# Kernel tuning notes

Hardware: AMD Instinct MI355X
Metric: run time of the kernel (lower is better)

The kernel has to match this reference:

```python
import math
import jax, jax.numpy as jnp
import numpy as np

NEG = -1e32
H = 8          # n_heads
L2 = 1e-05


def _ln(x, g, b):
    m = jnp.mean(x, -1, keepdims=True)
    v = jnp.mean((x - m) ** 2, -1, keepdims=True)
    return g * (x - m) * jax.lax.rsqrt(v + 1e-5) + b


def _attn(q, k, v, gam, mask_k, zero_pad):
    # q,k,v: [B,H,S,d]; monotonic distance-decay attention (AKT style)
    d_k = q.shape[-1]
    S = q.shape[2]
    scores = jnp.einsum('bhqd,bhkd->bhqk', q, k) / math.sqrt(d_k)
    # torch: triu(ones, k=mask)==0  ->  tril(0) if mask_k==1 else tril(-1)
    mask = jnp.tril(jnp.ones((S, S), bool), 0 if mask_k == 1 else -1)[None, None]
    # first (detached) softmax, used only to build the distance effect
    s_ = jax.nn.softmax(jnp.where(mask, scores, NEG), -1) * mask
    distcum = jnp.cumsum(s_, -1)
    disttot = jnp.sum(s_, -1, keepdims=True)
    idx = jnp.arange(S, dtype=jnp.float32)
    pos = jnp.abs(idx[None, :] - idx[:, None])[None, None]  # |j - i|
    dist = jax.lax.stop_gradient(
        jnp.sqrt(jnp.clip((disttot - distcum) * pos, 0.0, None)))
    gamma = -jax.nn.softplus(gam)[None]  # [1,H,1,1], gam is learned
    total_effect = jnp.clip(jnp.exp(dist * gamma), 1e-5, 1e5)
    scores = jax.nn.softmax(jnp.where(mask, scores * total_effect, NEG), -1)
    if zero_pad:
        scores = scores.at[:, :, 0, :].set(0.0)
    return jnp.einsum('bhqk,bhkd->bhqd', scores, v)


def _mha(qi, ki, vi, kW, kb, vW, vb, oW, ob, gam, mask_k, zero_pad):
    # kq_same=True: q and k both use k_linear
    B, S = qi.shape[:2]
    sp = lambda x: x.reshape(B, S, H, -1).transpose(0, 2, 1, 3)
    q = sp(qi @ kW + kb)
    k = sp(ki @ kW + kb)
    v = sp(vi @ vW + vb)
    o = _attn(q, k, v, gam, mask_k, zero_pad)
    o = o.transpose(0, 2, 1, 3).reshape(B, S, -1)
    return o @ oW + ob


def _tlayer(query, key, values, mask_k, zero_pad, apply_pos,
            kW, kb, vW, vb, oW, ob, gam, ln1g, ln1b,
            f1W, f1b, f2W, f2b, ln2g, ln2b):
    q2 = _mha(query, key, values, kW, kb, vW, vb, oW, ob, gam, mask_k, zero_pad)
    x = _ln(query + q2, ln1g, ln1b)
    if apply_pos:
        ff = jax.nn.relu(x @ f1W + f1b) @ f2W + f2b
        x = _ln(x + ff, ln2g, ln2b)
    return x


def _forward(p_data, pa_data, target, pemb_W, diff_W, qemb_W, qemb_b,
             y_kW, y_kb, y_vW, y_vb, y_oW, y_ob, y_gam, y_ln1g, y_ln1b,
             y_f1W, y_f1b, y_f2W, y_f2b, y_ln2g, y_ln2b,
             x_kW, x_kb, x_vW, x_vb, x_oW, x_ob, x_gam, x_ln1g, x_ln1b,
             h_kW, h_kb, h_vW, h_vb, h_oW, h_ob, h_gam, h_ln1g, h_ln1b,
             h_f1W, h_f1b, h_f2W, h_f2b, h_ln2g, h_ln2b,
             oln1g, oln1b, o1W, o1b, oln2g, oln2b, o2W, o2b,
             oln3g, oln3b, o3W, o3b):
    NPID = pemb_W.shape[0] - 1

    def qe(qd):  # q_embed: Linear -> ReLU, normalized by row-sum of q_data
        return jax.nn.relu(qd @ qemb_W + qemb_b) / jnp.sum(qd, -1, keepdims=True)

    q_data = jax.nn.sigmoid(pemb_W[p_data])           # [B,S,NQ+1]
    q_embed = qe(q_data)                              # [B,S,D]
    pa_pos = jnp.where(pa_data > NPID, pa_data - NPID, 0)
    pa_neg = jnp.where(pa_data <= NPID, pa_data, 0)
    qa_pos = jax.nn.sigmoid(pemb_W[pa_pos])
    qa_neg = jax.nn.sigmoid(pemb_W[pa_neg])
    qa_embed = jnp.concatenate([qe(qa_pos), qe(qa_neg)], -1)  # [B,S,2D]
    pid = diff_W[p_data]                              # [B,S,1]
    q_embed = q_embed + pid
    qa_embed = qa_embed + pid
    c_reg = jnp.sum(pid ** 2) * L2

    # Architecture (n_blocks = 1)
    y = _tlayer(qa_embed, qa_embed, qa_embed, 1, False, True,
                y_kW, y_kb, y_vW, y_vb, y_oW, y_ob, y_gam, y_ln1g, y_ln1b,
                y_f1W, y_f1b, y_f2W, y_f2b, y_ln2g, y_ln2b)
    x = _tlayer(q_embed, q_embed, q_embed, 1, False, False,
                x_kW, x_kb, x_vW, x_vb, x_oW, x_ob, x_gam, x_ln1g, x_ln1b,
                None, None, None, None, None, None)
    x = _tlayer(x, x, y, 0, True, True,
                h_kW, h_kb, h_vW, h_vb, h_oW, h_ob, h_gam, h_ln1g, h_ln1b,
                h_f1W, h_f1b, h_f2W, h_f2b, h_ln2g, h_ln2b)

    c = jnp.concatenate([x, q_embed], -1)             # [B,S,2D]
    o = jax.nn.relu(_ln(c, oln1g, oln1b) @ o1W + o1b)
    o = jax.nn.relu(_ln(o, oln2g, oln2b) @ o2W + o2b)
    out = _ln(o, oln3g, oln3b) @ o3W + o3b            # [B,S,1]
    return out, c_reg


def setup_inputs():
    B, S, D, NQ, NPID, FC, DFF = 8, 1024, 256, 1024, 4096, 512, 2048
    key = jax.random.key(0)
    cnt = [0]

    def nk():
        cnt[0] += 1
        return jax.random.fold_in(key, cnt[0])

    def nrm(shape, s=0.05):
        return jax.random.normal(nk(), shape, dtype=jnp.float32) * s

    z = lambda sh: jnp.zeros(sh, jnp.float32)
    on = lambda sh: jnp.ones(sh, jnp.float32)

    return dict(
        p_data=jax.random.randint(nk(), (B, S), 0, NPID + 1),
        pa_data=jax.random.randint(nk(), (B, S), 0, 2 * NPID + 1),
        target=jax.random.uniform(nk(), (B, S), jnp.float32),
        pemb_W=nrm((NPID + 1, NQ + 1), 1.0), diff_W=nrm((NPID + 1, 1), 0.1),
        qemb_W=nrm((NQ + 1, D)), qemb_b=z((D,)),
        y_kW=nrm((2 * D, 2 * D)), y_kb=z((2 * D,)),
        y_vW=nrm((2 * D, 2 * D)), y_vb=z((2 * D,)),
        y_oW=nrm((2 * D, 2 * D)), y_ob=z((2 * D,)), y_gam=nrm((H, 1, 1), 1.0),
        y_ln1g=on((2 * D,)), y_ln1b=z((2 * D,)),
        y_f1W=nrm((2 * D, DFF)), y_f1b=z((DFF,)),
        y_f2W=nrm((DFF, 2 * D)), y_f2b=z((2 * D,)),
        y_ln2g=on((2 * D,)), y_ln2b=z((2 * D,)),
        x_kW=nrm((D, D)), x_kb=z((D,)), x_vW=nrm((D, D)), x_vb=z((D,)),
        x_oW=nrm((D, D)), x_ob=z((D,)), x_gam=nrm((H, 1, 1), 1.0),
        x_ln1g=on((D,)), x_ln1b=z((D,)),
        h_kW=nrm((D, D)), h_kb=z((D,)),
        h_vW=nrm((2 * D, 2 * D)), h_vb=z((2 * D,)),
        h_oW=nrm((2 * D, D)), h_ob=z((D,)), h_gam=nrm((H, 1, 1), 1.0),
        h_ln1g=on((D,)), h_ln1b=z((D,)),
        h_f1W=nrm((D, DFF)), h_f1b=z((DFF,)),
        h_f2W=nrm((DFF, D)), h_f2b=z((D,)),
        h_ln2g=on((D,)), h_ln2b=z((D,)),
        oln1g=on((2 * D,)), oln1b=z((2 * D,)),
        o1W=nrm((2 * D, FC)), o1b=z((FC,)),
        oln2g=on((FC,)), oln2b=z((FC,)),
        o2W=nrm((FC, 256)), o2b=z((256,)),
        oln3g=on((256,)), oln3b=z((256,)),
        o3W=nrm((256, 1)), o3b=z((1,)),
    )


def reference(p_data, pa_data, target, pemb_W, diff_W, qemb_W, qemb_b,
              y_kW, y_kb, y_vW, y_vb, y_oW, y_ob, y_gam, y_ln1g, y_ln1b,
              y_f1W, y_f1b, y_f2W, y_f2b, y_ln2g, y_ln2b,
              x_kW, x_kb, x_vW, x_vb, x_oW, x_ob, x_gam, x_ln1g, x_ln1b,
              h_kW, h_kb, h_vW, h_vb, h_oW, h_ob, h_gam, h_ln1g, h_ln1b,
              h_f1W, h_f1b, h_f2W, h_f2b, h_ln2g, h_ln2b,
              oln1g, oln1b, o1W, o1b, oln2g, oln2b, o2W, o2b,
              oln3g, oln3b, o3W, o3b):
    return _forward(p_data, pa_data, target, pemb_W, diff_W, qemb_W, qemb_b,
                    y_kW, y_kb, y_vW, y_vb, y_oW, y_ob, y_gam, y_ln1g, y_ln1b,
                    y_f1W, y_f1b, y_f2W, y_f2b, y_ln2g, y_ln2b,
                    x_kW, x_kb, x_vW, x_vb, x_oW, x_ob, x_gam, x_ln1g, x_ln1b,
                    h_kW, h_kb, h_vW, h_vb, h_oW, h_ob, h_gam, h_ln1g, h_ln1b,
                    h_f1W, h_f1b, h_f2W, h_f2b, h_ln2g, h_ln2b,
                    oln1g, oln1b, o1W, o1b, oln2g, oln2b, o2W, o2b,
                    oln3g, oln3b, o3W, o3b)
```

## Files before the change

### kernel.cpp

```cpp
#include <hip/hip_runtime.h>
#include <hip/hip_bf16.h>
#include <math.h>

#define NHEADS 8
#define L2E 1.44269504f

typedef __attribute__((ext_vector_type(8))) __bf16 bfrag;
typedef __attribute__((ext_vector_type(4))) float f32x4;
typedef __attribute__((ext_vector_type(8))) unsigned short u16x8;

static __device__ __forceinline__ unsigned short f2bf(float f) {
  unsigned u = __float_as_uint(f);
  unsigned r = (u + 0x7fffu + ((u >> 16) & 1u)) >> 16;
  return (unsigned short)r;
}

static __device__ __forceinline__ void gload_lds16(const void* g, void* l) {
  __builtin_amdgcn_global_load_lds(
      (const __attribute__((address_space(1))) unsigned int*)g,
      (__attribute__((address_space(3))) unsigned int*)l, 16, 0, 0);
}

static __device__ __forceinline__ float block_reduce_sum(float v, float* red) {
  int t = threadIdx.x;
// ... 15 lines not shown
  int row = blockIdx.x;
  float s = 0.f;
  for (int k = threadIdx.x; k < Kp; k += 256) {
    float v = 0.f;
    if (k < Kd) {
      v = 1.f / (1.f + __expf(-Wp[(size_t)row * Kd + k]));
      s += v;
    }
    Sgb[(size_t)row * Kp + k] = f2bf(v);
  }
  float tot = block_reduce_sum(s, red);
  if (threadIdx.x == 0) Ssum[row] = tot;
}

struct TDesc { const float* src; unsigned short* dst; int K, N, Kp, tilesX, blk0; };
struct TPack { TDesc d[16]; };

__global__ __launch_bounds__(256) void tconv_all_kernel(TPack P) {
  __shared__ float t[32][33];
  int bid = blockIdx.x;
  int di = 0;
  #pragma unroll
  for (int k = 1; k < 16; ++k) if (bid >= P.d[k].blk0) di = k;
  const float* src = P.d[di].src;
  unsigned short* dst = P.d[di].dst;
  int K = P.d[di].K, N = P.d[di].N, Kp = P.d[di].Kp, tilesX = P.d[di].tilesX;
  int local = bid - P.d[di].blk0;
  int bn = (local % tilesX) * 32;
  int bk = (local / tilesX) * 32;
  int tid = threadIdx.x;
  int tx = tid & 31, ty = tid >> 5;
  #pragma unroll
  for (int u = 0; u < 4; ++u) {
    int k = bk + ty + u * 8, n = bn + tx;
    t[ty + u * 8][tx] = (k < K && n < N) ? src[(size_t)k * N + n] : 0.f;
  }
  __syncthreads();
  #pragma unroll
  for (int u = 0; u < 4; ++u) {
    int n = bn + ty + u * 8, kk = bk + tx;
    if (n < N && kk < Kp)
      dst[(size_t)n * Kp + kk] = f2bf(t[tx][ty + u * 8]);
  }
}

template<int BM, int EPI, bool WF32, bool WBF, bool WTR>
__global__ __launch_bounds__(256) void mgemm_kernel(
    const unsigned short* __restrict__ A, const unsigned short* __restrict__ Bt,
    const float* __restrict__ bias, float* __restrict__ C,
    unsigned short* __restrict__ Cb, unsigned short* __restrict__ Ct,
    int M, int N, int K, const float* __restrict__ divv,
    const float* __restrict__ bias2, int Nk)
{
  constexpr int NJ = (BM == 128) ? 4 : 2;
  constexpr bool SPLIT = WBF && WTR;
  __shared__ __align__(16) unsigned short Als[BM * 32];
  __shared__ __align__(16) unsigned short Bls[128 * 32];
  const int tid = threadIdx.x;
  const int lane = tid & 63, w = tid >> 6;
  const int wm = (BM == 128) ? (w >> 1) : 0;
  const int wn = (BM == 128) ? (w & 1) : w;
  const int brow = blockIdx.y * BM, bcol = blockIdx.x * 128;

  f32x4 acc[4][NJ] = {};

  for (int k0 = 0; k0 < K; k0 += 32) {
    #pragma unroll
    for (int q = 0; q < 2; ++q) {
      int s = w * 128 + q * 64 + lane;
      int r = s >> 2, g = s & 3;
      int gs = g ^ (r & 3);
      int gc = bcol + r; if (gc > N - 1) gc = N - 1;
      gload_lds16(Bt + (size_t)gc * K + k0 + gs * 8,
                  (char*)Bls + (w * 2048 + q * 1024));
    }
    if constexpr (BM == 128) {
      #pragma unroll
      for (int q = 0; q < 2; ++q) {
        int s = w * 128 + q * 64 + lane;
        int r = s >> 2, g = s & 3;
        int gs = g ^ (r & 3);
        int gr = brow + r; if (gr > M - 1) gr = M - 1;
        gload_lds16(A + (size_t)gr * K + k0 + gs * 8,
                    (char*)Als + (w * 2048 + q * 1024));
      }
    } else {
      int s = w * 64 + lane;
      int r = s >> 2, g = s & 3;
      int gs = g ^ (r & 3);
      int gr = brow + r; if (gr > M - 1) gr = M - 1;
      gload_lds16(A + (size_t)gr * K + k0 + gs * 8,
                  (char*)Als + w * 1024);
    }
    __syncthreads();

    bfrag av[4], bv[NJ];
    #pragma unroll
    for (int f = 0; f < 4; ++f) {
      int rA = wm * 64 + f * 16 + (lane & 15);
      av[f] = *(const bfrag*)((const char*)Als + rA * 64 + ((((lane >> 4) ^ (rA & 3))) << 4));
    }
    #pragma unroll
    for (int f = 0; f < NJ; ++f) {
      int rB = wn * (16 * NJ) + f * 16 + (lane & 15);
      bv[f] = *(const bfrag*)((const char*)Bls + rB * 64 + ((((lane >> 4) ^ (rB & 3))) << 4));
    }
    #pragma unroll
    for (int i = 0; i < 4; ++i)
      #pragma unroll
      for (int j = 0; j < NJ; ++j)
        acc[i][j] = __builtin_amdgcn_mfma_f32_16x16x32_bf16(av[i], bv[j], acc[i][j], 0, 0, 0);
    __syncthreads();
  }

  #pragma unroll
  for (int i = 0; i < 4; ++i) {
    int gr0 = brow + wm * 64 + i * 16 + (lane >> 4) * 4;
    #pragma unroll
    for (int j = 0; j < NJ; ++j) {
      int gc = bcol + wn * (16 * NJ) + j * 16 + (lane & 15);
      float bsv;
      if (SPLIT) bsv = (gc < Nk) ? bias[gc] : bias2[gc - Nk];
      else       bsv = bias ? bias[gc] : 0.f;
      float vv[4];
      #pragma unroll
      for (int q = 0; q < 4; ++q) {
        int gr = gr0 + q;
        float v = acc[i][j][q] + bsv;
        if (EPI >= 1) v = fmaxf(v, 0.f);
        if (EPI == 2) v = (gr < M) ? v / divv[gr] : v;
        vv[q] = v;
      }
      if (SPLIT) {
        if (gc < Nk) {
          #pragma unroll
          for (int q = 0; q < 4; ++q) {
            int gr = gr0 + q;
            if (gr < M) Cb[(size_t)gr * Nk + gc] = f2bf(vv[q]);
          }
        } else {
          ushort4 h4 = { f2bf(vv[0]), f2bf(vv[1]), f2bf(vv[2]), f2bf(vv[3]) };
          *(ushort4*)(Ct + (size_t)(gc - Nk) * M + gr0) = h4;
        }
      } else {
        #pragma unroll
        for (int q = 0; q < 4; ++q) {
          int gr = gr0 + q;
          if (gr >= M) continue;
          if (WF32) C[(size_t)gr * N + gc] = vv[q];
          if (WBF)  Cb[(size_t)gr * N + gc] = f2bf(vv[q]);
        }
        if (WTR) {
          ushort4 h4 = { f2bf(vv[0]), f2bf(vv[1]), f2bf(vv[2]), f2bf(vv[3]) };
          *(ushort4*)(Ct + (size_t)gc * M + gr0) = h4;
        }
      }
    }
  }
}

__global__ __launch_bounds__(256) void gather_kernel(
    const int* __restrict__ p_data, const int* __restrict__ pa_data,
    const float* __restrict__ E, const float* __restrict__ diff_W,
    float* __restrict__ qemb, unsigned short* __restrict__ qembb,
    float* __restrict__ qaemb, unsigned short* __restrict__ qaembb)
{
  int idx = blockIdx.x * 256 + threadIdx.x;
  if (idx >= 8192 * 512) return;
  int row = idx >> 9, c = idx & 511;
  int p = p_data[row];
  float pid = diff_W[p];
  if (c < 256) {
    float v = E[(size_t)p * 256 + c] + pid;
    qemb[(size_t)row * 256 + c] = v;
    qembb[(size_t)row * 256 + c] = f2bf(v);
  }
  int pa = pa_data[row];
  int ppos = (pa > 4096) ? pa - 4096 : 0;
  int pneg = (pa <= 4096) ? pa : 0;
  float v = (c < 256) ? E[(size_t)ppos * 256 + c] : E[(size_t)pneg * 256 + (c - 256)];
  v += pid;
  qaemb[(size_t)row * 512 + c] = v;
  qaembb[(size_t)row * 512 + c] = f2bf(v);
}

__global__ __launch_bounds__(256) void creg_kernel(
    const int* __restrict__ p_data, const float* __restrict__ dW,
    float* __restrict__ out)
{
  __shared__ float red[256];
  float s = 0.f;
  for (int i = threadIdx.x; i < 8192; i += 256) {
    float v = dW[p_data[i]];
    s += v * v;
  }
  float tot = block_reduce_sum(s, red);
  if (threadIdx.x == 0) out[0] = tot * 1e-5f;
}

template<int DK, int DV, int MASKK, int ZP, int CHUNK>
__global__ __launch_bounds__(512, 4) void attn7_kernel(
    const unsigned short* __restrict__ QKb, const unsigned short* __restrict__ Vt,
    const float* __restrict__ gamp, unsigned short* __restrict__ O,
    int S, int MT, int bxoff)
{
  constexpr int RS = 36 * CHUNK + 4;
  constexpr int LBITS = (CHUNK == 32) ? 2 : 1;
  constexpr int LM = (1 << LBITS) - 1;
  constexpr int HIOFF = 64 * CHUNK;
  constexpr int NPAR = (DV == 64) ? 2 : 4;
  constexpr int NFIN = (DV == 64) ? 4 : 2;
  constexpr int NP   = (DV == 32) ? 6 : 4;
  constexpr int MAXIT = (DV == 64) ? (CHUNK == 32 ? 8 : 4) : (CHUNK == 32 ? 4 : 2);
  const int DMK = NHEADS * DK, DMV = NHEADS * DV;
  const int nIb = gridDim.x;
  const int id = blockIdx.x + blockIdx.y * nIb;
  const int cpx = nIb * 8;
  const int W = (id & 7) * cpx + (id >> 3);
  const int ib = (nIb - 1) - (W % nIb);
  const int bh = W / nIb;
  const int i0 = (ib + bxoff) * 16;
  const int b = bh >> 3, h = bh & 7;
  const int tid = threadIdx.x;
  const int lane = tid & 63, w = tid >> 6;
  const size_t rowbase = (size_t)b * S;

  __shared__ __align__(16) float sc[16 * RS];
  __shared__ float red[NP * 16 * 17];
  __shared__ float wrow[16];

  const int jmaxBlk = MASKK ? (i0 + 15) : (i0 + 14);
  const int nT = jmaxBlk / 64 + 1;
  const int NK = nT * 64;

  const int qr = lane & 15;
  const int ko8 = (lane >> 4) * 8;
  const float rscale = rsqrtf((float)DK) * L2E;

  const int dblk = (DV == 64) ? (w & 3) : (w & 1);
  const int par  = (DV == 64) ? (w >> 2) : (w >> 1);
  const int dcol = h * DV + dblk * 16 + (lane & 15);
  const unsigned short* vrow = Vt + (size_t)dcol * MT + rowbase;
  bfrag vpre[2 * MAXIT];

  bfrag qf[DK / 32];
  #pragma unroll
  for (int ks = 0; ks < DK / 32; ++ks)
    qf[ks] = *(const bfrag*)(QKb + (rowbase + i0 + qr) * DMK + h * DK + ks * 32 + ko8);

  for (int t0 = 0; t0 < NK; t0 += 128) {
    int tt = t0 + (w >> 2) * 64;
    if (tt < NK) {
      int jb = tt + (w & 3) * 16 + qr;
      bfrag kf[DK / 32];
      #pragma unroll
      for (int ks = 0; ks < DK / 32; ++ks)
        kf[ks] = *(const bfrag*)(QKb + (rowbase + jb) * DMK + h * DK + ks * 32 + ko8);
      f32x4 accs = {};
      #pragma unroll
      for (int ks = 0; ks < DK / 32; ++ks)
        accs = __builtin_amdgcn_mfma_f32_16x16x32_bf16(qf[ks], kf[ks], accs, 0, 0, 0);
      int ja = jb + 4 * (jb >> 5);
      int r0 = (lane >> 4) * 4;
      #pragma unroll
      for (int q = 0; q < 4; ++q)
        sc[(r0 + q) * RS + ja] = accs[q] * rscale;
    }
  }
  __syncthreads();

  {
    const int g = tid >> 5, l = tid & 31;
    const int i = i0 + g;
    const int jmax = MASKK ? i : i - 1;
    const int jb0 = CHUNK * l;
    const int sb = g * RS + jb0 + 4 * (jb0 >> 5);

    float p[CHUNK];
    float m1 = -1e30f;
    #pragma unroll
    for (int c = 0; c < CHUNK / 4; ++c) {
      f32x4 v = *(const f32x4*)(sc + sb + c * 4);
      #pragma unroll
      for (int k = 0; k < 4; ++k) {
        int j = jb0 + c * 4 + k;
        float s = (j <= jmax) ? v[k] : -1e30f;
        p[c * 4 + k] = s;
        m1 = fmaxf(m1, s);
      }
    }
    #pragma unroll
    for (int o = 16; o > 0; o >>= 1) m1 = fmaxf(m1, __shfl_xor(m1, o, 32));

    float e1[CHUNK];
    float lloc = 0.f;
    #pragma unroll
    for (int t = 0; t < CHUNK; ++t) { e1[t] = __builtin_amdgcn_exp2f(p[t] - m1); lloc += e1[t]; }
    float l1 = lloc;
    #pragma unroll
    for (int o = 16; o > 0; o >>= 1) l1 += __shfl_xor(l1, o, 32);

    float scn = lloc;
    #pragma unroll
    for (int o = 1; o < 32; o <<= 1) {
      float u = __shfl_up(scn, o, 32);
      if (l >= o) scn += u;
    }
    float cum = scn - lloc;

    float gv = gamp[h];
    float sp = fmaxf(gv, 0.f) + log1pf(__expf(-fabsf(gv)));
    float gmr = -sp * L2E * rsqrtf(l1);
    float dj = (float)(i - jb0);
    float m2 = -1e30f;
    #pragma unroll
    for (int t = 0; t < CHUNK; ++t) {
      cum += e1[t];
      float rem = fmaxf(l1 - cum, 0.f);
      float dsq = sqrtf(rem * fabsf(dj));
      dj -= 1.f;
      float eff = fmaxf(__builtin_amdgcn_exp2f(gmr * dsq), 1e-5f);
      p[t] = p[t] * eff;
      m2 = fmaxf(m2, p[t]);
    }
    #pragma unroll
    for (int o = 16; o > 0; o >>= 1) m2 = fmaxf(m2, __shfl_xor(m2, o, 32));

    float l2 = 0.f;
    #pragma unroll
    for (int t = 0; t < CHUNK; ++t) { p[t] = __builtin_amdgcn_exp2f(p[t] - m2); l2 += p[t]; }
    #pragma unroll
    for (int o = 16; o > 0; o >>= 1) l2 += __shfl_xor(l2, o, 32);
    bool validrow = (jmax >= 0) && !(ZP && i == 0);
    float wgt = validrow ? (1.f / l2) : 0.f;
    if (l == 0) wrow[g] = wgt;

    #pragma unroll
    for (int it = 0; it < MAXIT; ++it) {
      int t0 = (par + it * NPAR) * 64;
      int t0c = (t0 < NK) ? t0 : 0;
      #pragma unroll
      for (int ks = 0; ks < 2; ++ks)
        vpre[it * 2 + ks] = *(const bfrag*)(vrow + t0c + ks * 32 + ko8);
    }

    char* rowB = (char*)sc + (size_t)g * (RS * 4);
    #pragma unroll
    for (int k = 0; k < CHUNK / 8; ++k) {
      int bb = (CHUNK / 8) * l + k;
      int pb = ((bb & LM) << 5) | (bb >> LBITS);
      u16x8 hi8, lo8;
      #pragma unroll
      for (int e = 0; e < 8; ++e) {
        float v = p[8 * k + e];
        __bf16 hb = (__bf16)v;
        hi8[e] = __builtin_bit_cast(unsigned short, hb);
        lo8[e] = __builtin_bit_cast(unsigned short, (__bf16)(v - (float)hb));
      }
      *(u16x8*)(rowB + 16 * pb) = hi8;
      *(u16x8*)(rowB + HIOFF + 16 * pb) = lo8;
    }
  }
  __syncthreads();

  f32x4 acco = {};
  const char* rowB = (const char*)sc + (size_t)qr * (RS * 4);
  #pragma unroll
  for (int it = 0; it < MAXIT; ++it) {
    int t0 = (par + it * NPAR) * 64;
    if (t0 < NK) {
      #pragma unroll
      for (int ks = 0; ks < 2; ++ks) {
        int jo = t0 + ks * 32 + ko8;
        int bb = jo >> 3;
        int pb = ((bb & LM) << 5) | (bb >> LBITS);
        bfrag ph = *(const bfrag*)(rowB + 16 * pb);
        bfrag pl = *(const bfrag*)(rowB + HIOFF + 16 * pb);
        bfrag vf = vpre[it * 2 + ks];
        acco = __builtin_amdgcn_mfma_f32_16x16x32_bf16(pl, vf, acco, 0, 0, 0);
        acco = __builtin_amdgcn_mfma_f32_16x16x32_bf16(ph, vf, acco, 0, 0, 0);
      }
    }
  }

  if (w >= NFIN) {
    #pragma unroll
    for (int q = 0; q < 4; ++q)
      red[(w - NFIN) * 272 + ((lane >> 4) * 4 + q) * 17 + (lane & 15)] = acco[q];
  }
  __syncthreads();
  if (w < NFIN) {
    for (int pp = w; pp < NP; pp += NFIN) {
      #pragma unroll
      for (int q = 0; q < 4; ++q)
        acco[q] += red[pp * 272 + ((lane >> 4) * 4 + q) * 17 + (lane & 15)];
    }
    int r0 = (lane >> 4) * 4;
    #pragma unroll
    for (int q = 0; q < 4; ++q) {
      float wv = wrow[r0 + q];
      O[(rowbase + i0 + r0 + q) * DMV + dcol] = f2bf(acco[q] * wv);
    }
  }
}

template<int D, bool WF, bool WB>
__global__ __launch_bounds__(256) void ln4_kernel(
    const float* __restrict__ X, const float* __restrict__ R,
    const float* __restrict__ g, const float* __restrict__ be,
    float* __restrict__ Y, unsigned short* __restrict__ Yb)
{
  constexpr int NC = D / 256;
  int row = blockIdx.x * 4 + (threadIdx.x >> 6);
  int lane = threadIdx.x & 63;
  const float* x = X + (size_t)row * D;
  f32x4 xv[NC];
  float s = 0.f;
  #pragma unroll
  for (int c = 0; c < NC; ++c) {
    xv[c] = *(const f32x4*)(x + c * 256 + lane * 4);
    if (R) {
      f32x4 rv = *(const f32x4*)(R + (size_t)row * D + c * 256 + lane * 4);
      #pragma unroll
      for (int k = 0; k < 4; ++k) xv[c][k] += rv[k];
    }
    #pragma unroll
    for (int k = 0; k < 4; ++k) s += xv[c][k];
  }
  #pragma unroll
  for (int o = 32; o > 0; o >>= 1) s += __shfl_xor(s, o, 64);
  float mean = s / (float)D;
  float vs = 0.f;
  #pragma unroll
  for (int c = 0; c < NC; ++c)
    #pragma unroll
    for (int k = 0; k < 4; ++k) { float d = xv[c][k] - mean; vs += d * d; }
  #pragma unroll
  for (int o = 32; o > 0; o >>= 1) vs += __shfl_xor(vs, o, 64);
  float rstd = rsqrtf(vs / (float)D + 1e-5f);
  #pragma unroll
  for (int c = 0; c < NC; ++c) {
    f32x4 gv = *(const f32x4*)(g + c * 256 + lane * 4);
    f32x4 bv = *(const f32x4*)(be + c * 256 + lane * 4);
    f32x4 ov;
    #pragma unroll
    for (int k = 0; k < 4; ++k) ov[k] = gv[k] * (xv[c][k] - mean) * rstd + bv[k];
    if (WF) *(f32x4*)(Y + (size_t)row * D + c * 256 + lane * 4) = ov;
    if (WB) {
// ... 167 lines not shown
  float* XO   = ws + oXO;   unsigned short* XOb = (unsigned short*)(ws + oXOb);
  float* HO   = ws + oHO;
  float* S0   = ws + oS0;
  unsigned short* S2b = (unsigned short*)(ws + oS2b);
  float* S3   = ws + oS3;
  float* S4   = ws + oS4;
  float* SX   = ws + oSX;   unsigned short* SXb = (unsigned short*)(ws + oSXb);
  unsigned short* S0b = (unsigned short*)(ws + oS0b);
  unsigned short* Vt  = (unsigned short*)(ws + oVt);
  unsigned short* FFb = (unsigned short*)S0;

  unsigned short* Wqe  = (unsigned short*)(ws + oWqe);
  unsigned short* Wyk  = (unsigned short*)(ws + oWyk);
  unsigned short* Wyv  = (unsigned short*)(ws + oWyv);
  unsigned short* Wyo  = (unsigned short*)(ws + oWyo);
  unsigned short* Wyf1 = (unsigned short*)(ws + oWyf1);
  unsigned short* Wyf2 = (unsigned short*)(ws + oWyf2);
  unsigned short* Wxk  = (unsigned short*)(ws + oWxk);
  unsigned short* Wxv  = (unsigned short*)(ws + oWxv);
  unsigned short* Wxo  = (unsigned short*)(ws + oWxo);
  unsigned short* Whk  = (unsigned short*)(ws + oWhk);
  unsigned short* Whv  = (unsigned short*)(ws + oWhv);
  unsigned short* Who  = (unsigned short*)(ws + oWho);
  unsigned short* Whf1 = (unsigned short*)(ws + oWhf1);
  unsigned short* Whf2 = (unsigned short*)(ws + oWhf2);
  unsigned short* Wo1  = (unsigned short*)(ws + oWo1);
  unsigned short* Wo2  = (unsigned short*)(ws + oWo2);

  dim3 blk(256);
  int nElem512 = (8192 * 512 + 255) / 256;

  {
    struct HD { const float* src; unsigned short* dst; int K, N, Kp; };
    const HD hd[16] = {
      {qemb_W, Wqe, KQ, 256, KQP},
      {y_kW, Wyk, 512, 512, 512}, {y_vW, Wyv, 512, 512, 512}, {y_oW, Wyo, 512, 512, 512},
      {y_f1W, Wyf1, 512, 2048, 512}, {y_f2W, Wyf2, 2048, 512, 2048},
      {x_kW, Wxk, 256, 256, 256}, {x_vW, Wxv, 256, 256, 256}, {x_oW, Wxo, 256, 256, 256},
      {h_kW, Whk, 256, 256, 256}, {h_vW, Whv, 512, 512, 512}, {h_oW, Who, 512, 256, 512},
      {h_f1W, Whf1, 256, 2048, 256}, {h_f2W, Whf2, 2048, 256, 2048},
      {o1W, Wo1, 512, 512, 512}, {o2W, Wo2, 512, 256, 512},
    };
    TPack P;
    int tot = 0;
    for (int k = 0; k < 16; ++k) {
      int tx = (hd[k].N + 31) / 32, ty = (hd[k].Kp + 31) / 32;
      P.d[k] = { hd[k].src, hd[k].dst, hd[k].K, hd[k].N, hd[k].Kp, tx, tot };
      tot += tx * ty;
    }
    tconv_all_kernel<<<dim3(tot), blk, 0, stream>>>(P);
  }

  auto gg128 = [](int Mm, int Nn) { return dim3((unsigned)(Nn / 128), (unsigned)((Mm + 127) / 128)); };
  auto gg64  = [](int Mm, int Nn) { return dim3((unsigned)(Nn / 128), (unsigned)((Mm + 63) / 64)); };

  sig_kernel<<<R, blk, 0, stream>>>(pemb_W, SIGb, SSUM, KQ, KQP);
  mgemm_kernel<64, 2, true, false, false><<<gg64(R, 256), blk, 0, stream>>>(SIGb, Wqe, qemb_b, E, nullptr, nullptr, R, 256, KQP, SSUM, nullptr, 0);
  gather_kernel<<<nElem512, blk, 0, stream>>>(p_data, pa_data, E, diff_W, QE, QEb, QA, QAb);
  creg_kernel<<<1, blk, 0, stream>>>(p_data, diff_W, out_f + 8192);

  dim3 ablk(512);
  dim3 lgrid(M / 4);
  dim3 agB(32, B * NHEADS), agC(32, B * NHEADS);

  mgemm_kernel<128, 0, false, true, true><<<dim3(8, 64), blk, 0, stream>>>(QAb, Wyk, y_kb, nullptr, S0b, Vt, M, 1024, 512, nullptr, y_vb, 512);
  attn7_kernel<64, 64, 1, 0, 16><<<agB, ablk, 0, stream>>>(S0b, Vt, y_gam, S2b, S, M, 0);
  attn7_kernel<64, 64, 1, 0, 32><<<agC, ablk, 0, stream>>>(S0b, Vt, y_gam, S2b, S, M, 32);
  mgemm_kernel<128, 0, true, false, false><<<gg128(M, 512), blk, 0, stream>>>(S2b, Wyo, y_ob, S3, nullptr, nullptr, M, 512, 512, nullptr, nullptr, 0);
  ln4_kernel<512, true, true><<<lgrid, blk, 0, stream>>>(QA, S3, y_ln1g, y_ln1b, SX, SXb);
  mgemm_kernel<128, 1, false, true, false><<<gg128(M, 2048), blk, 0, stream>>>(SXb, Wyf1, y_f1b, nullptr, FFb, nullptr, M, 2048, 512, nullptr, nullptr, 0);
  mgemm_kernel<128, 0, true, false, false><<<gg128(M, 512), blk, 0, stream>>>(FFb, Wyf2, y_f2b, S4, nullptr, nullptr, M, 512, 2048, nullptr, nullptr, 0);
  ln4_kernel<512, false, true><<<lgrid, blk, 0, stream>>>(SX, S4, y_ln2g, y_ln2b, nullptr, YOb);

  mgemm_kernel<128, 0, false, true, true><<<dim3(4, 64), blk, 0, stream>>>(QEb, Wxk, x_kb, nullptr, S0b, Vt, M, 512, 256, nullptr, x_vb, 256);
  attn7_kernel<32, 32, 1, 0, 16><<<agB, ablk, 0, stream>>>(S0b, Vt, x_gam, S2b, S, M, 0);
  attn7_kernel<32, 32, 1, 0, 32><<<agC, ablk, 0, stream>>>(S0b, Vt, x_gam, S2b, S, M, 32);
  mgemm_kernel<64, 0, true, false, false><<<gg64(M, 256), blk, 0, stream>>>(S2b, Wxo, x_ob, S3, nullptr, nullptr, M, 256, 256, nullptr, nullptr, 0);
  ln4_kernel<256, true, true><<<lgrid, blk, 0, stream>>>(QE, S3, x_ln1g, x_ln1b, XO, XOb);

  mgemm_kernel<64, 0, false, true, false><<<gg64(M, 256), blk, 0, stream>>>(XOb, Whk, h_kb, nullptr, S0b, nullptr, M, 256, 256, nullptr, nullptr, 0);
  mgemm_kernel<128, 0, false, false, true><<<gg128(M, 512), blk, 0, stream>>>(YOb, Whv, h_vb, nullptr, nullptr, Vt, M, 512, 512, nullptr, nullptr, 0);
  attn7_kernel<32, 64, 0, 1, 16><<<agB, ablk, 0, stream>>>(S0b, Vt, h_gam, S2b, S, M, 0);
  attn7_kernel<32, 64, 0, 1, 32><<<agC, ablk, 0, stream>>>(S0b, Vt, h_gam, S2b, S, M, 32);
  mgemm_kernel<64, 0, true, false, false><<<gg64(M, 256), blk, 0, stream>>>(S2b, Who, h_ob, S3, nullptr, nullptr, M, 256, 512, nullptr, nullptr, 0);
  ln4_kernel<256, true, true><<<lgrid, blk, 0, stream>>>(XO, S3, h_ln1g, h_ln1b, SX, SXb);
  mgemm_kernel<128, 1, false, true, false><<<gg128(M, 2048), blk, 0, stream>>>(SXb, Whf1, h_f1b, nullptr, FFb, nullptr, M, 2048, 256, nullptr, nullptr, 0);
  mgemm_kernel<64, 0, true, false, false><<<gg64(M, 256), blk, 0, stream>>>(FFb, Whf2, h_f2b, S4, nullptr, nullptr, M, 256, 2048, nullptr, nullptr, 0);
  ln4_kernel<256, true, false><<<lgrid, blk, 0, stream>>>(SX, S4, h_ln2g, h_ln2b, HO, nullptr);

  lnc_kernel<<<lgrid, blk, 0, stream>>>(HO, QE, oln1g, oln1b, SXb);
  mgemm_kernel<128, 1, true, false, false><<<gg128(M, 512), blk, 0, stream>>>(SXb, Wo1, o1b, S3, nullptr, nullptr, M, 512, 512, nullptr, nullptr, 0);
  ln4_kernel<512, false, true><<<lgrid, blk, 0, stream>>>(S3, nullptr, oln2g, oln2b, nullptr, SXb);
  mgemm_kernel<64, 1, true, false, false><<<gg64(M, 256), blk, 0, stream>>>(SXb, Wo2, o2b, S4, nullptr, nullptr, M, 256, 512, nullptr, nullptr, 0);
  lndot_kernel<<<lgrid, blk, 0, stream>>>(S4, oln3g, oln3b, o3W, o3b, out_f);
}
```

Measured before the change: 836.8 us.

## Widen attention blocks to 1024 threads with one wavefront per query row

The attention kernel moves from 512 to 1024 threads per block and assigns a full 64-lane wavefront to each query row, so wave-wide shuffles replace the 32-lane sub-group ones. The score pass and the P·V pass are split across twice as many waves, and the cross-partition reduction reuses the score shared buffer instead of a separate array. V fragments are now loaded inside the MFMA loop rather than prefetched before the softmax, which gives up that overlap in exchange for lower register pressure. The 1024-thread blocks and the extra barrier may reduce occupancy or add synchronization cost.

```diff
diff --git a/kernel.cpp b/kernel.cpp
--- a/kernel.cpp
+++ b/kernel.cpp
@@ -237,20 +237,20 @@
   if (threadIdx.x == 0) out[0] = tot * 1e-5f;
 }
 
-template<int DK, int DV, int MASKK, int ZP, int CHUNK>
-__global__ __launch_bounds__(512, 4) void attn7_kernel(
+template<int DK, int DV, int MASKK, int ZP, int CL>
+__global__ __launch_bounds__(1024, 8) void attn8_kernel(
     const unsigned short* __restrict__ QKb, const unsigned short* __restrict__ Vt,
     const float* __restrict__ gamp, unsigned short* __restrict__ O,
     int S, int MT, int bxoff)
 {
-  constexpr int RS = 36 * CHUNK + 4;
-  constexpr int LBITS = (CHUNK == 32) ? 2 : 1;
-  constexpr int LM = (1 << LBITS) - 1;
-  constexpr int HIOFF = 64 * CHUNK;
-  constexpr int NPAR = (DV == 64) ? 2 : 4;
-  constexpr int NFIN = (DV == 64) ? 4 : 2;
-  constexpr int NP   = (DV == 32) ? 6 : 4;
-  constexpr int MAXIT = (DV == 64) ? (CHUNK == 32 ? 8 : 4) : (CHUNK == 32 ? 4 : 2);
+  constexpr int CHUNK = CL / 64;
+  constexpr int RS = CL + CL / 8 + 4;
+  constexpr int NB = CL / 8;
+  constexpr int LSH = (NB == 128) ? 6 : 5;
+  constexpr int HIOFF = NB * 16;
+  constexpr int NPAR = (DV == 64) ? 4 : 8;
+  constexpr int NDB  = (DV == 64) ? 4 : 2;
+  constexpr int MAXIT = CL / (64 * NPAR);
   const int DMK = NHEADS * DK, DMV = NHEADS * DV;
   const int nIb = gridDim.x;
   const int id = blockIdx.x + blockIdx.y * nIb;
@@ -265,29 +265,21 @@
   const size_t rowbase = (size_t)b * S;
 
   __shared__ __align__(16) float sc[16 * RS];
-  __shared__ float red[NP * 16 * 17];
   __shared__ float wrow[16];
 
   const int jmaxBlk = MASKK ? (i0 + 15) : (i0 + 14);
-  const int nT = jmaxBlk / 64 + 1;
-  const int NK = nT * 64;
+  const int NK = (jmaxBlk / 64 + 1) * 64;
 
   const int qr = lane & 15;
   const int ko8 = (lane >> 4) * 8;
   const float rscale = rsqrtf((float)DK) * L2E;
 
-  const int dblk = (DV == 64) ? (w & 3) : (w & 1);
-  const int par  = (DV == 64) ? (w >> 2) : (w >> 1);
-  const int dcol = h * DV + dblk * 16 + (lane & 15);
-  const unsigned short* vrow = Vt + (size_t)dcol * MT + rowbase;
-  bfrag vpre[2 * MAXIT];
-
   bfrag qf[DK / 32];
   #pragma unroll
   for (int ks = 0; ks < DK / 32; ++ks)
     qf[ks] = *(const bfrag*)(QKb + (rowbase + i0 + qr) * DMK + h * DK + ks * 32 + ko8);
 
-  for (int t0 = 0; t0 < NK; t0 += 128) {
+  for (int t0 = 0; t0 < NK; t0 += 256) {
     int tt = t0 + (w >> 2) * 64;
     if (tt < NK) {
       int jb = tt + (w & 3) * 16 + qr;
@@ -309,7 +301,7 @@
   __syncthreads();
 
   {
-    const int g = tid >> 5, l = tid & 31;
+    const int g = w, l = lane;
     const int i = i0 + g;
     const int jmax = MASKK ? i : i - 1;
     const int jb0 = CHUNK * l;
@@ -329,7 +321,7 @@
       }
     }
     #pragma unroll
-    for (int o = 16; o > 0; o >>= 1) m1 = fmaxf(m1, __shfl_xor(m1, o, 32));
+    for (int o = 32; o > 0; o >>= 1) m1 = fmaxf(m1, __shfl_xor(m1, o, 64));
 
     float e1[CHUNK];
     float lloc = 0.f;
@@ -337,12 +329,12 @@
     for (int t = 0; t < CHUNK; ++t) { e1[t] = __builtin_amdgcn_exp2f(p[t] - m1); lloc += e1[t]; }
     float l1 = lloc;
     #pragma unroll
-    for (int o = 16; o > 0; o >>= 1) l1 += __shfl_xor(l1, o, 32);
+    for (int o = 32; o > 0; o >>= 1) l1 += __shfl_xor(l1, o, 64);
 
     float scn = lloc;
     #pragma unroll
-    for (int o = 1; o < 32; o <<= 1) {
-      float u = __shfl_up(scn, o, 32);
+    for (int o = 1; o < 64; o <<= 1) {
+      float u = __shfl_up(scn, o, 64);
       if (l >= o) scn += u;
     }
     float cum = scn - lloc;
@@ -363,31 +355,22 @@
       m2 = fmaxf(m2, p[t]);
     }
     #pragma unroll
-    for (int o = 16; o > 0; o >>= 1) m2 = fmaxf(m2, __shfl_xor(m2, o, 32));
+    for (int o = 32; o > 0; o >>= 1) m2 = fmaxf(m2, __shfl_xor(m2, o, 64));
 
     float l2 = 0.f;
     #pragma unroll
     for (int t = 0; t < CHUNK; ++t) { p[t] = __builtin_amdgcn_exp2f(p[t] - m2); l2 += p[t]; }
     #pragma unroll
-    for (int o = 16; o > 0; o >>= 1) l2 += __shfl_xor(l2, o, 32);
+    for (int o = 32; o > 0; o >>= 1) l2 += __shfl_xor(l2, o, 64);
     bool validrow = (jmax >= 0) && !(ZP && i == 0);
     float wgt = validrow ? (1.f / l2) : 0.f;
     if (l == 0) wrow[g] = wgt;
 
-    #pragma unroll
-    for (int it = 0; it < MAXIT; ++it) {
-      int t0 = (par + it * NPAR) * 64;
-      int t0c = (t0 < NK) ? t0 : 0;
-      #pragma unroll
-      for (int ks = 0; ks < 2; ++ks)
-        vpre[it * 2 + ks] = *(const bfrag*)(vrow + t0c + ks * 32 + ko8);
-    }
-
     char* rowB = (char*)sc + (size_t)g * (RS * 4);
     #pragma unroll
     for (int k = 0; k < CHUNK / 8; ++k) {
       int bb = (CHUNK / 8) * l + k;
-      int pb = ((bb & LM) << 5) | (bb >> LBITS);
+      int pb = ((bb & 1) << LSH) | (bb >> 1);
       u16x8 hi8, lo8;
       #pragma unroll
       for (int e = 0; e < 8; ++e) {
@@ -402,6 +385,10 @@
   }
   __syncthreads();
 
+  const int dblk = (DV == 64) ? (w & 3) : (w & 1);
+  const int par  = (DV == 64) ? (w >> 2) : (w >> 1);
+  const int dcol = h * DV + dblk * 16 + (lane & 15);
+  const unsigned short* vrow = Vt + (size_t)dcol * MT + rowbase;
   f32x4 acco = {};
   const char* rowB = (const char*)sc + (size_t)qr * (RS * 4);
   #pragma unroll
@@ -412,27 +399,32 @@
       for (int ks = 0; ks < 2; ++ks) {
         int jo = t0 + ks * 32 + ko8;
         int bb = jo >> 3;
-        int pb = ((bb & LM) << 5) | (bb >> LBITS);
+        int pb = ((bb & 1) << LSH) | (bb >> 1);
         bfrag ph = *(const bfrag*)(rowB + 16 * pb);
         bfrag pl = *(const bfrag*)(rowB + HIOFF + 16 * pb);
-        bfrag vf = vpre[it * 2 + ks];
+        bfrag vf = *(const bfrag*)(vrow + jo);
         acco = __builtin_amdgcn_mfma_f32_16x16x32_bf16(pl, vf, acco, 0, 0, 0);
         acco = __builtin_amdgcn_mfma_f32_16x16x32_bf16(ph, vf, acco, 0, 0, 0);
       }
     }
   }
-
-  if (w >= NFIN) {
+  __syncthreads();
+
+  float* redA = sc;
+  if (par != 0) {
+    int slot = (par - 1) * NDB + dblk;
     #pragma unroll
     for (int q = 0; q < 4; ++q)
-      red[(w - NFIN) * 272 + ((lane >> 4) * 4 + q) * 17 + (lane & 15)] = acco[q];
+      redA[slot * 272 + ((lane >> 4) * 4 + q) * 17 + (lane & 15)] = acco[q];
   }
   __syncthreads();
-  if (w < NFIN) {
-    for (int pp = w; pp < NP; pp += NFIN) {
+  if (par == 0) {
+    #pragma unroll
+    for (int pp = 1; pp < NPAR; ++pp) {
+      int slot = (pp - 1) * NDB + dblk;
       #pragma unroll
       for (int q = 0; q < 4; ++q)
-        acco[q] += red[pp * 272 + ((lane >> 4) * 4 + q) * 17 + (lane & 15)];
+        acco[q] += redA[slot * 272 + ((lane >> 4) * 4 + q) * 17 + (lane & 15)];
     }
     int r0 = (lane >> 4) * 4;
     #pragma unroll
@@ -713,13 +705,13 @@
   gather_kernel<<<nElem512, blk, 0, stream>>>(p_data, pa_data, E, diff_W, QE, QEb, QA, QAb);
   creg_kernel<<<1, blk, 0, stream>>>(p_data, diff_W, out_f + 8192);
 
-  dim3 ablk(512);
+  dim3 ablk(1024);
   dim3 lgrid(M / 4);
   dim3 agB(32, B * NHEADS), agC(32, B * NHEADS);
 
   mgemm_kernel<128, 0, false, true, true><<<dim3(8, 64), blk, 0, stream>>>(QAb, Wyk, y_kb, nullptr, S0b, Vt, M, 1024, 512, nullptr, y_vb, 512);
-  attn7_kernel<64, 64, 1, 0, 16><<<agB, ablk, 0, stream>>>(S0b, Vt, y_gam, S2b, S, M, 0);
-  attn7_kernel<64, 64, 1, 0, 32><<<agC, ablk, 0, stream>>>(S0b, Vt, y_gam, S2b, S, M, 32);
+  attn8_kernel<64, 64, 1, 0, 512><<<agB, ablk, 0, stream>>>(S0b, Vt, y_gam, S2b, S, M, 0);
+  attn8_kernel<64, 64, 1, 0, 1024><<<agC, ablk, 0, stream>>>(S0b, Vt, y_gam, S2b, S, M, 32);
   mgemm_kernel<128, 0, true, false, false><<<gg128(M, 512), blk, 0, stream>>>(S2b, Wyo, y_ob, S3, nullptr, nullptr, M, 512, 512, nullptr, nullptr, 0);
   ln4_kernel<512, true, true><<<lgrid, blk, 0, stream>>>(QA, S3, y_ln1g, y_ln1b, SX, SXb);
   mgemm_kernel<128, 1, false, true, false><<<gg128(M, 2048), blk, 0, stream>>>(SXb, Wyf1, y_f1b, nullptr, FFb, nullptr, M, 2048, 512, nullptr, nullptr, 0);
@@ -727,15 +719,15 @@
   ln4_kernel<512, false, true><<<lgrid, blk, 0, stream>>>(SX, S4, y_ln2g, y_ln2b, nullptr, YOb);
 
   mgemm_kernel<128, 0, false, true, true><<<dim3(4, 64), blk, 0, stream>>>(QEb, Wxk, x_kb, nullptr, S0b, Vt, M, 512, 256, nullptr, x_vb, 256);
-  attn7_kernel<32, 32, 1, 0, 16><<<agB, ablk, 0, stream>>>(S0b, Vt, x_gam, S2b, S, M, 0);
-  attn7_kernel<32, 32, 1, 0, 32><<<agC, ablk, 0, stream>>>(S0b, Vt, x_gam, S2b, S, M, 32);
+  attn8_kernel<32, 32, 1, 0, 512><<<agB, ablk, 0, stream>>>(S0b, Vt, x_gam, S2b, S, M, 0);
+  attn8_kernel<32, 32, 1, 0, 1024><<<agC, ablk, 0, stream>>>(S0b, Vt, x_gam, S2b, S, M, 32);
   mgemm_kernel<64, 0, true, false, false><<<gg64(M, 256), blk, 0, stream>>>(S2b, Wxo, x_ob, S3, nullptr, nullptr, M, 256, 256, nullptr, nullptr, 0);
   ln4_kernel<256, true, true><<<lgrid, blk, 0, stream>>>(QE, S3, x_ln1g, x_ln1b, XO, XOb);
 
   mgemm_kernel<64, 0, false, true, false><<<gg64(M, 256), blk, 0, stream>>>(XOb, Whk, h_kb, nullptr, S0b, nullptr, M, 256, 256, nullptr, nullptr, 0);
   mgemm_kernel<128, 0, false, false, true><<<gg128(M, 512), blk, 0, stream>>>(YOb, Whv, h_vb, nullptr, nullptr, Vt, M, 512, 512, nullptr, nullptr, 0);
-  attn7_kernel<32, 64, 0, 1, 16><<<agB, ablk, 0, stream>>>(S0b, Vt, h_gam, S2b, S, M, 0);
-  attn7_kernel<32, 64, 0, 1, 32><<<agC, ablk, 0, stream>>>(S0b, Vt, h_gam, S2b, S, M, 32);
+  attn8_kernel<32, 64, 0, 1, 512><<<agB, ablk, 0, stream>>>(S0b, Vt, h_gam, S2b, S, M, 0);
+  attn8_kernel<32, 64, 0, 1, 1024><<<agC, ablk, 0, stream>>>(S0b, Vt, h_gam, S2b, S, M, 32);
   mgemm_kernel<64, 0, true, false, false><<<gg64(M, 256), blk, 0, stream>>>(S2b, Who, h_ob, S3, nullptr, nullptr, M, 256, 512, nullptr, nullptr, 0);
   ln4_kernel<256, true, true><<<lgrid, blk, 0, stream>>>(XO, S3, h_ln1g, h_ln1b, SX, SXb);
   mgemm_kernel<128, 1, false, true, false><<<gg128(M, 2048), blk, 0, stream>>>(SXb, Whf1, h_f1b, nullptr, FFb, nullptr, M, 2048, 256, nullptr, nullptr, 0);
```

After: 844.2 us. About the same (+0.9%).

## Use 64x64 GEMM tiles and cut attention register pressure for higher occupancy

Applied to the files above, without the earlier changes.

The BM=64 GEMM variant now uses a 64x64 tile with a 2x2 warp grid instead of 64x128, doubling the grid size for the N=256 GEMMs. The attention kernel drops the e1[] array (recomputing exp2) and the V prefetch registers, loads V inside the loop, and reuses the score shared buffer for the cross-warp reduction. This lets it declare 8 waves-per-SIMD occupancy for CHUNK=16. The aim is more resident blocks and better latency hiding, paid for with extra exp2 work and V loads that are no longer prefetched.

```diff
diff --git a/kernel.cpp b/kernel.cpp
--- a/kernel.cpp
+++ b/kernel.cpp
@@ -91,29 +91,31 @@
     int M, int N, int K, const float* __restrict__ divv,
     const float* __restrict__ bias2, int Nk)
 {
-  constexpr int NJ = (BM == 128) ? 4 : 2;
+  constexpr int TN  = (BM == 128) ? 128 : 64;
+  constexpr int NI  = (BM == 128) ? 4 : 2;
+  constexpr int NJ  = (BM == 128) ? 4 : 2;
+  constexpr int WSM = (BM == 128) ? 64 : 32;
   constexpr bool SPLIT = WBF && WTR;
   __shared__ __align__(16) unsigned short Als[BM * 32];
-  __shared__ __align__(16) unsigned short Bls[128 * 32];
+  __shared__ __align__(16) unsigned short Bls[TN * 32];
   const int tid = threadIdx.x;
   const int lane = tid & 63, w = tid >> 6;
-  const int wm = (BM == 128) ? (w >> 1) : 0;
-  const int wn = (BM == 128) ? (w & 1) : w;
-  const int brow = blockIdx.y * BM, bcol = blockIdx.x * 128;
-
-  f32x4 acc[4][NJ] = {};
+  const int wm = w >> 1, wn = w & 1;
+  const int brow = blockIdx.y * BM, bcol = blockIdx.x * TN;
+
+  f32x4 acc[NI][NJ] = {};
 
   for (int k0 = 0; k0 < K; k0 += 32) {
-    #pragma unroll
-    for (int q = 0; q < 2; ++q) {
-      int s = w * 128 + q * 64 + lane;
-      int r = s >> 2, g = s & 3;
-      int gs = g ^ (r & 3);
-      int gc = bcol + r; if (gc > N - 1) gc = N - 1;
-      gload_lds16(Bt + (size_t)gc * K + k0 + gs * 8,
-                  (char*)Bls + (w * 2048 + q * 1024));
-    }
     if constexpr (BM == 128) {
+      #pragma unroll
+      for (int q = 0; q < 2; ++q) {
+        int s = w * 128 + q * 64 + lane;
+        int r = s >> 2, g = s & 3;
+        int gs = g ^ (r & 3);
+        int gc = bcol + r; if (gc > N - 1) gc = N - 1;
+        gload_lds16(Bt + (size_t)gc * K + k0 + gs * 8,
+                    (char*)Bls + (w * 2048 + q * 1024));
+      }
       #pragma unroll
       for (int q = 0; q < 2; ++q) {
         int s = w * 128 + q * 64 + lane;
@@ -124,28 +126,38 @@
                     (char*)Als + (w * 2048 + q * 1024));
       }
     } else {
-      int s = w * 64 + lane;
-      int r = s >> 2, g = s & 3;
-      int gs = g ^ (r & 3);
-      int gr = brow + r; if (gr > M - 1) gr = M - 1;
-      gload_lds16(A + (size_t)gr * K + k0 + gs * 8,
-                  (char*)Als + w * 1024);
+      {
+        int s = tid;
+        int r = s >> 2, g = s & 3;
+        int gs = g ^ (r & 3);
+        int gc = bcol + r; if (gc > N - 1) gc = N - 1;
+        gload_lds16(Bt + (size_t)gc * K + k0 + gs * 8,
+                    (char*)Bls + w * 1024);
+      }
+      {
+        int s = tid;
+        int r = s >> 2, g = s & 3;
+        int gs = g ^ (r & 3);
+        int gr = brow + r; if (gr > M - 1) gr = M - 1;
+        gload_lds16(A + (size_t)gr * K + k0 + gs * 8,
+                    (char*)Als + w * 1024);
+      }
     }
     __syncthreads();
 
-    bfrag av[4], bv[NJ];
-    #pragma unroll
-    for (int f = 0; f < 4; ++f) {
-      int rA = wm * 64 + f * 16 + (lane & 15);
+    bfrag av[NI], bv[NJ];
+    #pragma unroll
+    for (int f = 0; f < NI; ++f) {
+      int rA = wm * WSM + f * 16 + (lane & 15);
       av[f] = *(const bfrag*)((const char*)Als + rA * 64 + ((((lane >> 4) ^ (rA & 3))) << 4));
     }
     #pragma unroll
     for (int f = 0; f < NJ; ++f) {
-      int rB = wn * (16 * NJ) + f * 16 + (lane & 15);
+      int rB = wn * WSM + f * 16 + (lane & 15);
       bv[f] = *(const bfrag*)((const char*)Bls + rB * 64 + ((((lane >> 4) ^ (rB & 3))) << 4));
     }
     #pragma unroll
-    for (int i = 0; i < 4; ++i)
+    for (int i = 0; i < NI; ++i)
       #pragma unroll
       for (int j = 0; j < NJ; ++j)
         acc[i][j] = __builtin_amdgcn_mfma_f32_16x16x32_bf16(av[i], bv[j], acc[i][j], 0, 0, 0);
@@ -153,11 +165,11 @@
   }
 
   #pragma unroll
-  for (int i = 0; i < 4; ++i) {
-    int gr0 = brow + wm * 64 + i * 16 + (lane >> 4) * 4;
+  for (int i = 0; i < NI; ++i) {
+    int gr0 = brow + wm * WSM + i * 16 + (lane >> 4) * 4;
     #pragma unroll
     for (int j = 0; j < NJ; ++j) {
-      int gc = bcol + wn * (16 * NJ) + j * 16 + (lane & 15);
+      int gc = bcol + wn * WSM + j * 16 + (lane & 15);
       float bsv;
       if (SPLIT) bsv = (gc < Nk) ? bias[gc] : bias2[gc - Nk];
       else       bsv = bias ? bias[gc] : 0.f;
@@ -238,7 +250,7 @@
 }
 
 template<int DK, int DV, int MASKK, int ZP, int CHUNK>
-__global__ __launch_bounds__(512, 4) void attn7_kernel(
+__global__ __launch_bounds__(512, (CHUNK == 16) ? 8 : 4) void attn9_kernel(
     const unsigned short* __restrict__ QKb, const unsigned short* __restrict__ Vt,
     const float* __restrict__ gamp, unsigned short* __restrict__ O,
     int S, int MT, int bxoff)
@@ -250,7 +262,6 @@
   constexpr int NPAR = (DV == 64) ? 2 : 4;
   constexpr int NFIN = (DV == 64) ? 4 : 2;
   constexpr int NP   = (DV == 32) ? 6 : 4;
-  constexpr int MAXIT = (DV == 64) ? (CHUNK == 32 ? 8 : 4) : (CHUNK == 32 ? 4 : 2);
   const int DMK = NHEADS * DK, DMV = NHEADS * DV;
   const int nIb = gridDim.x;
   const int id = blockIdx.x + blockIdx.y * nIb;
@@ -265,22 +276,14 @@
   const size_t rowbase = (size_t)b * S;
 
   __shared__ __align__(16) float sc[16 * RS];
-  __shared__ float red[NP * 16 * 17];
   __shared__ float wrow[16];
 
   const int jmaxBlk = MASKK ? (i0 + 15) : (i0 + 14);
-  const int nT = jmaxBlk / 64 + 1;
-  const int NK = nT * 64;
+  const int NK = (jmaxBlk / 64 + 1) * 64;
 
   const int qr = lane & 15;
   const int ko8 = (lane >> 4) * 8;
   const float rscale = rsqrtf((float)DK) * L2E;
-
-  const int dblk = (DV == 64) ? (w & 3) : (w & 1);
-  const int par  = (DV == 64) ? (w >> 2) : (w >> 1);
-  const int dcol = h * DV + dblk * 16 + (lane & 15);
-  const unsigned short* vrow = Vt + (size_t)dcol * MT + rowbase;
-  bfrag vpre[2 * MAXIT];
 
   bfrag qf[DK / 32];
   #pragma unroll
@@ -331,10 +334,9 @@
     #pragma unroll
     for (int o = 16; o > 0; o >>= 1) m1 = fmaxf(m1, __shfl_xor(m1, o, 32));
 
-    float e1[CHUNK];
     float lloc = 0.f;
     #pragma unroll
-    for (int t = 0; t < CHUNK; ++t) { e1[t] = __builtin_amdgcn_exp2f(p[t] - m1); lloc += e1[t]; }
+    for (int t = 0; t < CHUNK; ++t) lloc += __builtin_amdgcn_exp2f(p[t] - m1);
     float l1 = lloc;
     #pragma unroll
     for (int o = 16; o > 0; o >>= 1) l1 += __shfl_xor(l1, o, 32);
@@ -354,7 +356,7 @@
     float m2 = -1e30f;
     #pragma unroll
     for (int t = 0; t < CHUNK; ++t) {
-      cum += e1[t];
+      cum += __builtin_amdgcn_exp2f(p[t] - m1);
       float rem = fmaxf(l1 - cum, 0.f);
       float dsq = sqrtf(rem * fabsf(dj));
       dj -= 1.f;
@@ -373,15 +375,6 @@
     bool validrow = (jmax >= 0) && !(ZP && i == 0);
     float wgt = validrow ? (1.f / l2) : 0.f;
     if (l == 0) wrow[g] = wgt;
-
-    #pragma unroll
-    for (int it = 0; it < MAXIT; ++it) {
-      int t0 = (par + it * NPAR) * 64;
-      int t0c = (t0 < NK) ? t0 : 0;
-      #pragma unroll
-      for (int ks = 0; ks < 2; ++ks)
-        vpre[it * 2 + ks] = *(const bfrag*)(vrow + t0c + ks * 32 + ko8);
-    }
 
     char* rowB = (char*)sc + (size_t)g * (RS * 4);
     #pragma unroll
@@ -402,37 +395,40 @@
   }
   __syncthreads();
 
+  const int dblk = (DV == 64) ? (w & 3) : (w & 1);
+  const int par  = (DV == 64) ? (w >> 2) : (w >> 1);
+  const int dcol = h * DV + dblk * 16 + (lane & 15);
+  const unsigned short* vrow = Vt + (size_t)dcol * MT + rowbase;
   f32x4 acco = {};
   const char* rowB = (const char*)sc + (size_t)qr * (RS * 4);
-  #pragma unroll
-  for (int it = 0; it < MAXIT; ++it) {
-    int t0 = (par + it * NPAR) * 64;
-    if (t0 < NK) {
-      #pragma unroll
-      for (int ks = 0; ks < 2; ++ks) {
-        int jo = t0 + ks * 32 + ko8;
-        int bb = jo >> 3;
-        int pb = ((bb & LM) << 5) | (bb >> LBITS);
-        bfrag ph = *(const bfrag*)(rowB + 16 * pb);
-        bfrag pl = *(const bfrag*)(rowB + HIOFF + 16 * pb);
-        bfrag vf = vpre[it * 2 + ks];
-        acco = __builtin_amdgcn_mfma_f32_16x16x32_bf16(pl, vf, acco, 0, 0, 0);
-        acco = __builtin_amdgcn_mfma_f32_16x16x32_bf16(ph, vf, acco, 0, 0, 0);
-      }
-    }
-  }
-
+  for (int t0 = par * 64; t0 < NK; t0 += NPAR * 64) {
+    #pragma unroll
+    for (int ks = 0; ks < 2; ++ks) {
+      int jo = t0 + ks * 32 + ko8;
+      int bb = jo >> 3;
+      int pb = ((bb & LM) << 5) | (bb >> LBITS);
+      bfrag ph = *(const bfrag*)(rowB + 16 * pb);
+      bfrag pl = *(const bfrag*)(rowB + HIOFF + 16 * pb);
+      bfrag vf = *(const bfrag*)(vrow + jo);
+      acco = __builtin_amdgcn_mfma_f32_16x16x32_bf16(pl, vf, acco, 0, 0, 0);
+      acco = __builtin_amdgcn_mfma_f32_16x16x32_bf16(ph, vf, acco, 0, 0, 0);
+    }
+  }
+  __syncthreads();
+
+  float* redA = sc;
   if (w >= NFIN) {
+    int slot = w - NFIN;
     #pragma unroll
     for (int q = 0; q < 4; ++q)
-      red[(w - NFIN) * 272 + ((lane >> 4) * 4 + q) * 17 + (lane & 15)] = acco[q];
+      redA[slot * 272 + ((lane >> 4) * 4 + q) * 17 + (lane & 15)] = acco[q];
   }
   __syncthreads();
   if (w < NFIN) {
     for (int pp = w; pp < NP; pp += NFIN) {
       #pragma unroll
       for (int q = 0; q < 4; ++q)
-        acco[q] += red[pp * 272 + ((lane >> 4) * 4 + q) * 17 + (lane & 15)];
+        acco[q] += redA[pp * 272 + ((lane >> 4) * 4 + q) * 17 + (lane & 15)];
     }
     int r0 = (lane >> 4) * 4;
     #pragma unroll
@@ -706,7 +702,7 @@
   }
 
   auto gg128 = [](int Mm, int Nn) { return dim3((unsigned)(Nn / 128), (unsigned)((Mm + 127) / 128)); };
-  auto gg64  = [](int Mm, int Nn) { return dim3((unsigned)(Nn / 128), (unsigned)((Mm + 63) / 64)); };
+  auto gg64  = [](int Mm, int Nn) { return dim3((unsigned)(Nn / 64), (unsigned)((Mm + 63) / 64)); };
 
   sig_kernel<<<R, blk, 0, stream>>>(pemb_W, SIGb, SSUM, KQ, KQP);
   mgemm_kernel<64, 2, true, false, false><<<gg64(R, 256), blk, 0, stream>>>(SIGb, Wqe, qemb_b, E, nullptr, nullptr, R, 256, KQP, SSUM, nullptr, 0);
@@ -718,8 +714,8 @@
   dim3 agB(32, B * NHEADS), agC(32, B * NHEADS);
 
   mgemm_kernel<128, 0, false, true, true><<<dim3(8, 64), blk, 0, stream>>>(QAb, Wyk, y_kb, nullptr, S0b, Vt, M, 1024, 512, nullptr, y_vb, 512);
-  attn7_kernel<64, 64, 1, 0, 16><<<agB, ablk, 0, stream>>>(S0b, Vt, y_gam, S2b, S, M, 0);
-  attn7_kernel<64, 64, 1, 0, 32><<<agC, ablk, 0, stream>>>(S0b, Vt, y_gam, S2b, S, M, 32);
+  attn9_kernel<64, 64, 1, 0, 16><<<agB, ablk, 0, stream>>>(S0b, Vt, y_gam, S2b, S, M, 0);
+  attn9_kernel<64, 64, 1, 0, 32><<<agC, ablk, 0, stream>>>(S0b, Vt, y_gam, S2b, S, M, 32);
   mgemm_kernel<128, 0, true, false, false><<<gg128(M, 512), blk, 0, stream>>>(S2b, Wyo, y_ob, S3, nullptr, nullptr, M, 512, 512, nullptr, nullptr, 0);
   ln4_kernel<512, true, true><<<lgrid, blk, 0, stream>>>(QA, S3, y_ln1g, y_ln1b, SX, SXb);
   mgemm_kernel<128, 1, false, true, false><<<gg128(M, 2048), blk, 0, stream>>>(SXb, Wyf1, y_f1b, nullptr, FFb, nullptr, M, 2048, 512, nullptr, nullptr, 0);
@@ -727,15 +723,15 @@
   ln4_kernel<512, false, true><<<lgrid, blk, 0, stream>>>(SX, S4, y_ln2g, y_ln2b, nullptr, YOb);
 
   mgemm_kernel<128, 0, false, true, true><<<dim3(4, 64), blk, 0, stream>>>(QEb, Wxk, x_kb, nullptr, S0b, Vt, M, 512, 256, nullptr, x_vb, 256);
-  attn7_kernel<32, 32, 1, 0, 16><<<agB, ablk, 0, stream>>>(S0b, Vt, x_gam, S2b, S, M, 0);
-  attn7_kernel<32, 32, 1, 0, 32><<<agC, ablk, 0, stream>>>(S0b, Vt, x_gam, S2b, S, M, 32);
+  attn9_kernel<32, 32, 1, 0, 16><<<agB, ablk, 0, stream>>>(S0b, Vt, x_gam, S2b, S, M, 0);
+  attn9_kernel<32, 32, 1, 0, 32><<<agC, ablk, 0, stream>>>(S0b, Vt, x_gam, S2b, S, M, 32);
   mgemm_kernel<64, 0, true, false, false><<<gg64(M, 256), blk, 0, stream>>>(S2b, Wxo, x_ob, S3, nullptr, nullptr, M, 256, 256, nullptr, nullptr, 0);
   ln4_kernel<256, true, true><<<lgrid, blk, 0, stream>>>(QE, S3, x_ln1g, x_ln1b, XO, XOb);
 
   mgemm_kernel<64, 0, false, true, false><<<gg64(M, 256), blk, 0, stream>>>(XOb, Whk, h_kb, nullptr, S0b, nullptr, M, 256, 256, nullptr, nullptr, 0);
   mgemm_kernel<128, 0, false, false, true><<<gg128(M, 512), blk, 0, stream>>>(YOb, Whv, h_vb, nullptr, nullptr, Vt, M, 512, 512, nullptr, nullptr, 0);
-  attn7_kernel<32, 64, 0, 1, 16><<<agB, ablk, 0, stream>>>(S0b, Vt, h_gam, S2b, S, M, 0);
-  attn7_kernel<32, 64, 0, 1, 32><<<agC, ablk, 0, stream>>>(S0b, Vt, h_gam, S2b, S, M, 32);
+  attn9_kernel<32, 64, 0, 1, 16><<<agB, ablk, 0, stream>>>(S0b, Vt, h_gam, S2b, S, M, 0);
+  attn9_kernel<32, 64, 0, 1, 32><<<agC, ablk, 0, stream>>>(S0b, Vt, h_gam, S2b, S, M, 32);
   mgemm_kernel<64, 0, true, false, false><<<gg64(M, 256), blk, 0, stream>>>(S2b, Who, h_ob, S3, nullptr, nullptr, M, 256, 512, nullptr, nullptr, 0);
   ln4_kernel<256, true, true><<<lgrid, blk, 0, stream>>>(XO, S3, h_ln1g, h_ln1b, SX, SXb);
   mgemm_kernel<128, 1, false, true, false><<<gg128(M, 2048), blk, 0, stream>>>(SXb, Whf1, h_f1b, nullptr, FFb, nullptr, M, 2048, 256, nullptr, nullptr, 0);
```

New measurement: 787.5 us. 1.06x faster.
